# Kernel optimization log

Measured on AMD Instinct MI355X. Metric: run time of the kernel, lower is better.

The kernel has to match this reference:

```python
import jax, jax.numpy as jnp
import numpy as np

BS, NCAM, CIN, H, W = 1, 6, 512, 32, 88
MID = 256
DBINS = 112  # (58 - 2) / 0.5
VX, VY, VZ = 128, 128, 16


def conv2d(x, w, pad=1):
    return jax.lax.conv_general_dilated(
        x, w, (1, 1), [(pad, pad), (pad, pad)],
        dimension_numbers=('NCHW', 'OIHW', 'NCHW'))


def grid_sample_3d(feat, grid):
    """F.grid_sample 3D, bilinear, padding_mode='zeros', align_corners=False.
    feat: (N, C, D, H, W); grid: (N, X, Y, Z, 3) with xyz -> (W, H, D) coords in [-1,1].
    Returns (N, C, X, Y, Z)."""
    N, C, D, Hh, Ww = feat.shape
    gx, gy, gz = grid[..., 0], grid[..., 1], grid[..., 2]
    ix = ((gx + 1.0) * Ww - 1.0) * 0.5
    iy = ((gy + 1.0) * Hh - 1.0) * 0.5
    iz = ((gz + 1.0) * D - 1.0) * 0.5
    ix0, iy0, iz0 = jnp.floor(ix), jnp.floor(iy), jnp.floor(iz)
    fx, fy, fz = ix - ix0, iy - iy0, iz - iz0
    feat_flat = feat.reshape(N, C, D * Hh * Ww)
    out = jnp.zeros((N, C) + grid.shape[1:-1], feat.dtype)
    for dz in (0, 1):
        for dy in (0, 1):
            for dx in (0, 1):
                xi, yi, zi = ix0 + dx, iy0 + dy, iz0 + dz
                w_ = ((fx if dx else 1.0 - fx) * (fy if dy else 1.0 - fy)
                      * (fz if dz else 1.0 - fz))
                valid = ((xi >= 0) & (xi < Ww) & (yi >= 0) & (yi < Hh)
                         & (zi >= 0) & (zi < D))
                xc = jnp.clip(xi, 0, Ww - 1).astype(jnp.int32)
                yc = jnp.clip(yi, 0, Hh - 1).astype(jnp.int32)
                zc = jnp.clip(zi, 0, D - 1).astype(jnp.int32)
                idx = ((zc * Hh + yc) * Ww + xc).reshape(N, 1, -1)
                g = jnp.take_along_axis(feat_flat, idx, axis=2)
                g = g.reshape((N, C) + grid.shape[1:-1])
                out = out + g * (w_ * valid)[:, None]
    return out


def setup_inputs():
    key = jax.random.key(0)
    ks = jax.random.split(key, 16)
    f32 = jnp.float32
    img_feat = jax.random.normal(ks[0], (BS, NCAM, CIN, H, W), f32)
    intr = np.zeros((NCAM, 4, 4), np.float32)
    for i in range(NCAM):
        f = 1266.0 + 10.0 * i
        intr[i, 0, 0] = f; intr[i, 1, 1] = f
        intr[i, 0, 2] = 800.0; intr[i, 1, 2] = 450.0
        intr[i, 2, 2] = 1.0; intr[i, 3, 3] = 1.0
    intrins = jnp.asarray(intr)[None]  # (1, 6, 4, 4)
    # normalized frustum-sample coords; slightly beyond [-1,1] to hit zero padding
    grid = jax.random.uniform(ks[1], (BS, NCAM, VX, VY, VZ, 3), f32, -1.1, 1.1)
    s3 = (2.0 / (CIN * 9)) ** 0.5
    sm = (2.0 / (MID * 9)) ** 0.5
    s1 = (2.0 / MID) ** 0.5
    red_w = jax.random.normal(ks[2], (MID, CIN, 3, 3), f32) * s3
    red_s = jnp.ones((MID,), f32); red_b = jnp.zeros((MID,), f32)
    mlp_w1 = jax.random.normal(ks[3], (1, MID), f32) * 1.4
    mlp_b1 = jnp.zeros((MID,), f32)
    mlp_w2 = jax.random.normal(ks[4], (MID, MID), f32) * s1
    mlp_b2 = jnp.zeros((MID,), f32)
    se_rw = jax.random.normal(ks[5], (MID, MID, 1, 1), f32) * s1
    se_rb = jnp.zeros((MID,), f32)
    se_ew = jax.random.normal(ks[6], (MID, MID, 1, 1), f32) * s1
    se_eb = jnp.zeros((MID,), f32)
    bb_w = jax.random.normal(ks[7], (3, 2, MID, MID, 3, 3), f32) * sm
    bb_s = jnp.ones((3, 2, MID), f32); bb_b = jnp.zeros((3, 2, MID), f32)
    dp_w = jax.random.normal(ks[8], (DBINS, MID, 1, 1), f32) * s1
    dp_b = jnp.zeros((DBINS,), f32)
    return dict(img_feat=img_feat, intrins=intrins, grid=grid,
                red_w=red_w, red_s=red_s, red_b=red_b,
                mlp_w1=mlp_w1, mlp_b1=mlp_b1, mlp_w2=mlp_w2, mlp_b2=mlp_b2,
                se_rw=se_rw, se_rb=se_rb, se_ew=se_ew, se_eb=se_eb,
                bb_w=bb_w, bb_s=bb_s, bb_b=bb_b, dp_w=dp_w, dp_b=dp_b)


def reference(img_feat, intrins, grid, red_w, red_s, red_b,
              mlp_w1, mlp_b1, mlp_w2, mlp_b2,
              se_rw, se_rb, se_ew, se_eb, bb_w, bb_s, bb_b, dp_w, dp_b):
    bs, n, c, h, w = img_feat.shape
    x = img_feat.reshape(bs * n, c, h, w)
    # pixel-size SE conditioning from inverse intrinsics
    inv = jnp.linalg.inv(intrins)
    pixel_size = jnp.linalg.norm(
        jnp.stack([inv[..., 0, 0], inv[..., 1, 1]], -1), axis=-1).reshape(-1, 1)
    sp = pixel_size * 1000.0  # scale_depth_factor
    # reduce_conv: conv3x3 + (folded) BN + ReLU
    x = conv2d(x, red_w)
    x = jax.nn.relu(x * red_s[:, None, None] + red_b[:, None, None])
    # Mlp on scaled pixel size
    x_se = jax.nn.relu(sp @ mlp_w1 + mlp_b1) @ mlp_w2 + mlp_b2
    x_se = x_se[:, :, None, None]
    # SELayer
    t = jax.nn.relu(conv2d(x_se, se_rw, pad=0) + se_rb[:, None, None])
    gate = jax.nn.sigmoid(conv2d(t, se_ew, pad=0) + se_eb[:, None, None])
    x = x * gate
    # 3 BasicBlocks (conv-bn-relu-conv-bn + residual, relu), BN folded (eval)
    for i in range(3):
        y = conv2d(x, bb_w[i, 0])
        y = jax.nn.relu(y * bb_s[i, 0][:, None, None] + bb_b[i, 0][:, None, None])
        y = conv2d(y, bb_w[i, 1])
        y = y * bb_s[i, 1][:, None, None] + bb_b[i, 1][:, None, None]
        x = jax.nn.relu(x + y)
    depth = conv2d(x, dp_w, pad=0) + dp_b[:, None, None]  # (bs*n, D, h, w)
    dp = jax.nn.softmax(depth, axis=1)
    # stack depth prob and ones so one grid_sample yields features AND voxel mask
    feat = jnp.stack([dp, jnp.ones_like(dp)], axis=1)  # (bs*n, 2, D, h, w)
    g = grid.reshape((bs * n,) + grid.shape[2:])       # (bs*n, X, Y, Z, 3)
    sampled = grid_sample_3d(feat, g)                  # (bs*n, 2, X, Y, Z)
    sampled = sampled.reshape((bs, n) + sampled.shape[1:]).sum(axis=1)
    agg, masks = sampled[:, :1], sampled[:, 1:]
    out = jnp.where(masks > 0, agg / jnp.where(masks > 0, masks, 1.0), agg)
    return out  # (bs, 1, X, Y, Z)
```

## Files before the change

### kernel.cpp

```cpp
#include <hip/hip_runtime.h>

typedef _Float16 f16;
typedef _Float16 f16x8 __attribute__((ext_vector_type(8)));
typedef _Float16 f16x4 __attribute__((ext_vector_type(4)));
typedef float f32x4 __attribute__((ext_vector_type(4)));

#define NCAM 6
#define CINF 512
#define MIDC 256
#define DB   112
#define HH   32
#define WW   88
#define PH   34
#define PW   90
#define NPOS (HH*WW)

#define O_GATE   0L
#define O_WFRED  6144L
#define O_LOG    6144L
#define O_WFBB   2365440L
#define O_WFDP   9443328L
#define O_XP0    9508864L
#define O_X1     28309504L
#define O_DP     28309504L
#define O_X2     37709824L
#define O_X3     47110144L

__device__ __forceinline__ void gl_lds16(const void* g, void* l) {
  __builtin_amdgcn_global_load_lds((const __attribute__((address_space(1))) void*)g,
                                   (__attribute__((address_space(3))) void*)l, 16, 0, 0);
}

__global__ void halo_zero_kernel(f16* __restrict__ xp0, f16* __restrict__ X1,
                                 f16* __restrict__ X2, f16* __restrict__ X3) {
  int idx = blockIdx.x * 256 + threadIdx.x;
  f16* base; int C, rem;
  if (idx < 93696) { base = xp0; C = 512; rem = idx; }
  else {
    int k = idx - 93696;
    int bsel = k / 46848;
    if (bsel >= 3) return;
    rem = k - bsel * 46848; C = 256;
    base = (bsel == 0) ? X1 : (bsel == 1) ? X2 : X3;
  }
  int chunks = C >> 3;
  int cell = rem / chunks, cc = rem - cell * chunks;
  int cam = cell / 244, p = cell - cam * 244;
  int hh, ww;
  if (p < 90)       { hh = 0;  ww = p; }
  else if (p < 180) { hh = 33; ww = p - 90; }
  else { int q = p - 180; hh = 1 + (q >> 1); ww = (q & 1) * 89; }
  long o = ((long)(cam * PH + hh) * PW + ww) * C + cc * 8;
  f16x8 z = {0,0,0,0,0,0,0,0};
  *(f16x8*)(base + o) = z;
}

__global__ void wfrag_kernel(const float* __restrict__ src, const float* __restrict__ scale,
                             f16* __restrict__ dst, int NC, int G, int TAPS, int CI, int CO_SRC,
                             long per, long total) {
  long i = (long)blockIdx.x * blockDim.x + threadIdx.x;
  long stride = (long)gridDim.x * blockDim.x;
  int KST = CI >> 5;
  for (; i < total; i += stride) {
    int conv = (int)(i / per);
    long rem = i - (long)conv * per;
    int j = (int)(rem & 7);
    int lane = (int)((rem >> 3) & 63);
    int mi = (int)((rem >> 9) & 3);
    long b = rem >> 11;
    int ks = (int)(b % KST);
    long b2 = b / KST;
    int tap = (int)(b2 % TAPS);
    int g = (int)(b2 / TAPS);
    int co = g * 64 + mi * 16 + (lane & 15);
    int ci = ks * 32 + (lane >> 4) * 8 + j;
    float v = 0.f;
    if (co < CO_SRC) {
      v = src[(long)conv * CO_SRC * CI * TAPS + ((long)co * CI + ci) * TAPS + tap];
      if (scale) v *= scale[conv * CO_SRC + co];
    }
    dst[i] = (f16)v;
  }
}

__global__ void img_trans_kernel(const float* __restrict__ src, f16* __restrict__ dst) {
  __shared__ float tile[32][33];
  int tx = threadIdx.x & 31, ty = threadIdx.x >> 5;
  int wt = blockIdx.x % 3, ct = blockIdx.x / 3;
  int h = blockIdx.y, n = blockIdx.z;
  int w0 = wt * 32, c0 = ct * 32;
  #pragma unroll
  for (int i = 0; i < 4; ++i) {
    int cl = ty + i * 8;
    int w = w0 + tx;
    float v = 0.f;
    if (w < WW) v = src[((long)(n * CINF + c0 + cl) * HH + h) * WW + w];
    tile[cl][tx] = v;
  }
  __syncthreads();
  #pragma unroll
  for (int i = 0; i < 4; ++i) {
    int wl = ty + i * 8;
    int w = w0 + wl;
    if (w < WW)
      dst[((long)((n * PH + h + 1) * PW + (w + 1))) * CINF + c0 + tx] = (f16)tile[tx][wl];
  }
}

__global__ void se_gate_kernel(const float* __restrict__ intr,
                               const float* __restrict__ w1, const float* __restrict__ b1,
                               const float* __restrict__ w2, const float* __restrict__ b2,
                               const float* __restrict__ rw, const float* __restrict__ rb,
                               const float* __restrict__ ew, const float* __restrict__ eb,
                               float* __restrict__ gate) {
  __shared__ float sps;
  __shared__ float h1[MIDC];
  __shared__ float h2[MIDC];
  __shared__ float tt[MIDC];
  int n = blockIdx.x, c = threadIdx.x;
  if (c == 0) {
    float a[4][8];
    for (int i = 0; i < 4; ++i)
      for (int j = 0; j < 4; ++j) {
        a[i][j] = intr[n * 16 + i * 4 + j];
        a[i][4 + j] = (i == j) ? 1.f : 0.f;
      }
    for (int col = 0; col < 4; ++col) {
      int piv = col;
      for (int r2 = col + 1; r2 < 4; ++r2)
        if (fabsf(a[r2][col]) > fabsf(a[piv][col])) piv = r2;
      if (piv != col)
        for (int j = 0; j < 8; ++j) { float tv = a[col][j]; a[col][j] = a[piv][j]; a[piv][j] = tv; }
      float invp = 1.f / a[col][col];
      for (int j = 0; j < 8; ++j) a[col][j] *= invp;
      for (int r2 = 0; r2 < 4; ++r2)
        if (r2 != col) {
          float f = a[r2][col];
          for (int j = 0; j < 8; ++j) a[r2][j] -= f * a[col][j];
        }
    }
    float i00 = a[0][4], i11 = a[1][5];
    sps = sqrtf(i00 * i00 + i11 * i11) * 1000.f;
  }
  __syncthreads();
  float sp = sps;
  h1[c] = fmaxf(sp * w1[c] + b1[c], 0.f);
  __syncthreads();
  float acc = b2[c];
  for (int j = 0; j < MIDC; ++j) acc += h1[j] * w2[j * MIDC + c];
  h2[c] = acc;
  __syncthreads();
  acc = rb[c];
  for (int j = 0; j < MIDC; ++j) acc += rw[c * MIDC + j] * h2[j];
  tt[c] = fmaxf(acc, 0.f);
  __syncthreads();
  acc = eb[c];
  for (int j = 0; j < MIDC; ++j) acc += ew[c * MIDC + j] * tt[j];
  gate[n * MIDC + c] = 1.f / (1.f + expf(-acc));
}

template<int MODE, int CIN_T, int TAPS>
__global__ __launch_bounds__(256, 2)
void conv_mfma(const f16* __restrict__ X, const f16* __restrict__ Wf,
               const float* __restrict__ bias, const float* __restrict__ gate,
               const f16* __restrict__ res, f16* __restrict__ Yf16,
               float* __restrict__ Yf32, int co_tiles) {
  constexpr int KST = CIN_T / 32;
  constexpr int CPT = CIN_T / 64;
  constexpr int NCH = TAPS * CPT;
  constexpr int LCPT = (CPT == 8) ? 3 : 2;
  constexpr long GSTR = (long)TAPS * KST * 4096;
  constexpr int BSTR = 26624;
  __shared__ __align__(16) char S[2 * BSTR];

  const int t = threadIdx.x;
  const int wv = t >> 6, ln = t & 63, lm = ln & 15, quad = ln >> 4;
  const int wm = wv >> 1, wn = wv & 1;
  const int bid0 = blockIdx.x;
  const int cpx = gridDim.x >> 3;
  const int bid = (bid0 & 7) * cpx + (bid0 >> 3);
  const int co_tile = bid >> 8;
  const int r = bid & 255;
  int pbase, nrows;
  if (r < 224) { pbase = r * 64;               nrows = 64; }
  else         { pbase = 14336 + (r - 224) * 80; nrows = 80; }
  const int cam = pbase / NPOS;
  const int p0 = pbase - cam * NPOS;
  const int ntk = nrows >> 4;
  const int nregs = nrows >> 3;
  const int nti = (ntk + 1 - wn) >> 1;

  const f16* gB[3]; int ldsoffB[3];
  const int clog = (ln & 7) ^ (ln >> 3);
  #pragma unroll
  for (int j = 0; j < 3; ++j) {
    int reg = j * 4 + wv;
    int pl = p0 + reg * 8 + (ln >> 3);
    int hh = pl / WW, w2 = pl - hh * WW;
    gB[j] = X + ((long)((cam * PH + hh + 1) * PW + (w2 + 1))) * CIN_T + clog * 8;
    ldsoffB[j] = 16384 + reg * 1024;
  }

  const int sx0 = ((0 * 4 + quad) ^ (lm & 7)) * 16;
  const int sx1 = ((1 * 4 + quad) ^ (lm & 7)) * 16;

  f32x4 acc[4][3];
  #pragma unroll
  for (int mi = 0; mi < 4; ++mi)
    #pragma unroll
    for (int i = 0; i < 3; ++i)
      #pragma unroll
      for (int q = 0; q < 4; ++q) acc[mi][i][q] = 0.f;

  auto choff = [&](int c) -> long {
    long off = 0;
    if (TAPS == 9) {
      int tp = c >> LCPT;
      int dy = tp / 3 - 1, dx = tp % 3 - 1;
      off = (long)(dy * PW + dx) * CIN_T;
    }
    return off + (long)(c & (CPT - 1)) * 64;
  };
  auto stageA = [&](int bsel, int c) {
    const char* sb = (const char*)Wf + (long)c * 8192 + (long)ln * 16;
    char* db = S + bsel * BSTR;
    #pragma unroll
    for (int j = 0; j < 4; ++j) {
      int seg = j * 4 + wv;
      long gb = (long)(co_tile * 2 + (seg >> 3)) * GSTR;
      gl_lds16(sb + gb + (seg & 7) * 1024, db + seg * 1024);
    }
  };
  auto stageB = [&](int bsel, long curf) {
    #pragma unroll
    for (int j = 0; j < 3; ++j)
      if (j * 4 + wv < nregs)
        gl_lds16(gB[j] + curf, S + bsel * BSTR + ldsoffB[j]);
  };
  auto compute = [&](int bsel) {
    const char* ab = S + bsel * BSTR + wm * 8192 + ln * 16;
    const char* bb = S + bsel * BSTR + 16384 + lm * 128;
    #pragma unroll
    for (int s = 0; s < 2; ++s) {
      f16x8 af[4];
      #pragma unroll
      for (int mi = 0; mi < 4; ++mi)
        af[mi] = *(const f16x8*)(ab + s * 4096 + mi * 1024);
      int sx = s ? sx1 : sx0;
      #pragma unroll
      for (int i = 0; i < 3; ++i) {
        if (i < nti) {
          f16x8 bf = *(const f16x8*)(bb + (2 * i + wn) * 2048 + sx);
          #pragma unroll
          for (int mi = 0; mi < 4; ++mi)
            acc[mi][i] = __builtin_amdgcn_mfma_f32_16x16x32_f16(af[mi], bf, acc[mi][i], 0, 0, 0);
        }
      }
    }
  };

  stageA(0, 0);
  stageB(0, choff(0));
  __syncthreads();

  #pragma unroll 1
  for (int c = 0; c < NCH; ++c) {
    int cur = c & 1;
    if (c + 1 < NCH) { stageA(cur ^ 1, c + 1); stageB(cur ^ 1, choff(c + 1)); }
    compute(cur);
    __syncthreads();
  }

  float4 b4[4], g4[4];
  bool skip[4];
  #pragma unroll
  for (int mi = 0; mi < 4; ++mi) {
    int co_l = wm * 64 + mi * 16 + quad * 4;
    int co_g = co_tile * 128 + co_l;
    skip[mi] = (MODE == 3) && (co_l >= DB);
    if (!skip[mi]) b4[mi] = *(const float4*)(bias + co_g);
    if (MODE == 0) g4[mi] = *(const float4*)(gate + cam * MIDC + co_g);
  }
  #pragma unroll
  for (int i = 0; i < 3; ++i) {
    if (i >= nti) continue;
    int k = 2 * i + wn;
    int pos_l = p0 + k * 16 + lm;
    long ob;
    if (MODE == 3) ob = ((long)(cam * NPOS + pos_l)) * DB;
    else {
      int hh = pos_l / WW, w2 = pos_l - hh * WW;
      ob = ((long)((cam * PH + hh + 1) * PW + (w2 + 1))) * MIDC + co_tile * 128;
    }
    #pragma unroll
    for (int mi = 0; mi < 4; ++mi) {
      if (skip[mi]) continue;
      int co_l = wm * 64 + mi * 16 + quad * 4;
      float v[4];
      #pragma unroll
      for (int q = 0; q < 4; ++q) {
        float y = acc[mi][i][q];
        y += ((float*)&b4[mi])[q];
        if (MODE == 0) y = fmaxf(y, 0.f) * ((float*)&g4[mi])[q];
        else if (MODE == 1) y = fmaxf(y, 0.f);
        v[q] = y;
      }
      if (MODE == 3) {
        float4 o; o.x = v[0]; o.y = v[1]; o.z = v[2]; o.w = v[3];
        *(float4*)(Yf32 + ob + co_l) = o;
      } else if (MODE == 2) {
        f16x4 rv = *(const f16x4*)(res + ob + co_l);
        f16x4 o;
        #pragma unroll
        for (int q = 0; q < 4; ++q) o[q] = (f16)fmaxf(v[q] + (float)rv[q], 0.f);
        *(f16x4*)(Yf16 + ob + co_l) = o;
      } else {
        f16x4 o;
        #pragma unroll
        for (int q = 0; q < 4; ++q) o[q] = (f16)v[q];
        *(f16x4*)(Yf16 + ob + co_l) = o;
      }
    }
  }
}

__global__ void softmax_kernel(const float* __restrict__ L, float* __restrict__ dp) {
  int wid = (int)(((long)blockIdx.x * blockDim.x + threadIdx.x) >> 6);
  int lane = threadIdx.x & 63;
  if (wid >= NCAM * NPOS) return;
  const float* lp = L + (long)wid * DB;
  float v0 = -1e30f, v1 = -1e30f;
  if (lane < 56) { v0 = lp[lane * 2]; v1 = lp[lane * 2 + 1]; }
  float m = fmaxf(v0, v1);
  #pragma unroll
  for (int o = 32; o; o >>= 1) m = fmaxf(m, __shfl_xor(m, o));
  float e0 = 0.f, e1 = 0.f;
  if (lane < 56) { e0 = __expf(v0 - m); e1 = __expf(v1 - m); }
  float ssum = e0 + e1;
  #pragma unroll
  for (int o = 32; o; o >>= 1) ssum += __shfl_xor(ssum, o);
  float inv = 1.f / ssum;
  if (lane < 56) {
    float2 r; r.x = e0 * inv; r.y = e1 * inv;
    *(float2*)(dp + (long)wid * DB + lane * 2) = r;
  }
}

__global__ void sample_kernel(const float* __restrict__ grid, const float* __restrict__ dp,
                              float* __restrict__ out) {
  int v = blockIdx.x * blockDim.x + threadIdx.x;
  if (v >= 128 * 128 * 16) return;
  int vz = v & 15, vy = (v >> 4) & 127, vx = v >> 11;
  float agg = 0.f, msk = 0.f;
  #pragma unroll 1
  for (int n = 0; n < NCAM; ++n) {
    long gb = ((long)((n * 128 + vx) * 128 + vy) * 16 + vz) * 3;
    float gx = grid[gb], gy = grid[gb + 1], gz = grid[gb + 2];
    float ix = ((gx + 1.f) * (float)WW - 1.f) * 0.5f;
    float iy = ((gy + 1.f) * (float)HH - 1.f) * 0.5f;
    float iz = ((gz + 1.f) * (float)DB - 1.f) * 0.5f;
    float xf = floorf(ix), yf = floorf(iy), zf = floorf(iz);
    float fx = ix - xf, fy = iy - yf, fz = iz - zf;
    int x0 = (int)xf, y0 = (int)yf, z0 = (int)zf;
    float wxa[2] = {1.f - fx, fx};
    float wya[2] = {1.f - fy, fy};
    float wza[2] = {1.f - fz, fz};
    #pragma unroll
    for (int dy2 = 0; dy2 < 2; ++dy2) {
      int y = y0 + dy2;
      bool vyb = (y >= 0) && (y < HH);
      int yc = y < 0 ? 0 : (y > HH - 1 ? HH - 1 : y);
      #pragma unroll
      for (int dx2 = 0; dx2 < 2; ++dx2) {
        int x = x0 + dx2;
        bool vxb = (x >= 0) && (x < WW);
        int xc = x < 0 ? 0 : (x > WW - 1 ? WW - 1 : x);
        float wxy = wxa[dx2] * wya[dy2];
        const float* base = dp + ((long)((n * HH + yc) * WW + xc)) * DB;
        #pragma unroll
        for (int dz2 = 0; dz2 < 2; ++dz2) {
          int z = z0 + dz2;
          bool vzb = (z >= 0) && (z < DB);
          int zc = z < 0 ? 0 : (z > DB - 1 ? DB - 1 : z);
          float wgt = wxy * wza[dz2];
          if (vxb && vyb && vzb) {
            msk += wgt;
            agg += wgt * base[zc];
          }
        }
      }
    }
  }
  out[v] = (msk > 0.f) ? (agg / msk) : agg;
}

extern "C" void kernel_launch(void* const* d_in, const int* in_sizes, int n_in,
                              void* d_out, int out_size, void* d_ws, size_t ws_size,
                              hipStream_t stream) {
  const float* img   = (const float*)d_in[0];
  const float* intr  = (const float*)d_in[1];
  const float* grid  = (const float*)d_in[2];
  const float* red_w = (const float*)d_in[3];
  const float* red_s = (const float*)d_in[4];
  const float* red_b = (const float*)d_in[5];
  const float* w1    = (const float*)d_in[6];
  const float* b1    = (const float*)d_in[7];
  const float* w2    = (const float*)d_in[8];
  const float* b2    = (const float*)d_in[9];
  const float* rw    = (const float*)d_in[10];
  const float* rb    = (const float*)d_in[11];
  const float* ew    = (const float*)d_in[12];
  const float* eb    = (const float*)d_in[13];
  const float* bb_w  = (const float*)d_in[14];
  const float* bb_s  = (const float*)d_in[15];
  const float* bb_b  = (const float*)d_in[16];
  const float* dp_w  = (const float*)d_in[17];
  const float* dp_b  = (const float*)d_in[18];
  float* out = (float*)d_out;

  char* ws = (char*)d_ws;
  float* gate = (float*)(ws + O_GATE);
  f16* wfred  = (f16*)(ws + O_WFRED);
  f16* wfbb   = (f16*)(ws + O_WFBB);
  f16* wfdp   = (f16*)(ws + O_WFDP);
  f16* xp0    = (f16*)(ws + O_XP0);
  f16* X1     = (f16*)(ws + O_X1);
  f16* X2     = (f16*)(ws + O_X2);
  f16* X3     = (f16*)(ws + O_X3);
  float* Lg   = (float*)(ws + O_LOG);
  float* dpb  = (float*)(ws + O_DP);

  halo_zero_kernel<<<915, 256, 0, stream>>>(xp0, X1, X2, X3);
  {
    long per = 4L * 9 * 16 * 2048, total = per;
    wfrag_kernel<<<2048, 256, 0, stream>>>(red_w, red_s, wfred, 1, 4, 9, 512, 256, per, total);
  }
  {
    long per = 4L * 9 * 8 * 2048, total = 6 * per;
    wfrag_kernel<<<4096, 256, 0, stream>>>(bb_w, bb_s, wfbb, 6, 4, 9, 256, 256, per, total);
  }
  {
    long per = 2L * 1 * 8 * 2048, total = per;
    wfrag_kernel<<<128, 256, 0, stream>>>(dp_w, nullptr, wfdp, 1, 2, 1, 256, 112, per, total);
  }
  img_trans_kernel<<<dim3(48, 32, 6), 256, 0, stream>>>(img, xp0);
  se_gate_kernel<<<6, 256, 0, stream>>>(intr, w1, b1, w2, b2, rw, rb, ew, eb, gate);

  const long WCH = 4L * 9 * 8 * 2048;

  conv_mfma<0, 512, 9><<<512, 256, 0, stream>>>(xp0, wfred, red_b, gate, nullptr, X1, nullptr, 2);

  conv_mfma<1, 256, 9><<<512, 256, 0, stream>>>(X1, wfbb + 0 * WCH, bb_b + 0 * 256, nullptr, nullptr, X2, nullptr, 2);
  conv_mfma<2, 256, 9><<<512, 256, 0, stream>>>(X2, wfbb + 1 * WCH, bb_b + 1 * 256, nullptr, X1, X3, nullptr, 2);
  conv_mfma<1, 256, 9><<<512, 256, 0, stream>>>(X3, wfbb + 2 * WCH, bb_b + 2 * 256, nullptr, nullptr, X2, nullptr, 2);
  conv_mfma<2, 256, 9><<<512, 256, 0, stream>>>(X2, wfbb + 3 * WCH, bb_b + 3 * 256, nullptr, X3, X1, nullptr, 2);
  conv_mfma<1, 256, 9><<<512, 256, 0, stream>>>(X1, wfbb + 4 * WCH, bb_b + 4 * 256, nullptr, nullptr, X2, nullptr, 2);
  conv_mfma<2, 256, 9><<<512, 256, 0, stream>>>(X2, wfbb + 5 * WCH, bb_b + 5 * 256, nullptr, X1, X3, nullptr, 2);

  conv_mfma<3, 256, 1><<<256, 256, 0, stream>>>(X3, wfdp, dp_b, nullptr, nullptr, nullptr, Lg, 1);

  softmax_kernel<<<4224, 256, 0, stream>>>(Lg, dpb);
  sample_kernel<<<1024, 256, 0, stream>>>(grid, dpb, out);
}
```

Baseline: 492.2 us.

## Double conv pixel tile to 128-144 rows and halve grid size

Grows each conv block's pixel tile from 64/80 rows to 128/144 rows, so every weight tile staged in LDS is reused across twice as many output positions. Block count is halved and co_tile/row indexing is reordered so that both channel tiles of the same pixel tile are adjacent. The accumulator array grows to 4x5, and the launch-bounds occupancy hint is dropped. The cost is more registers and LDS per block, and with 256 blocks on 256 CUs only one block per CU, which leaves less latency hiding.

Result: slower. 526.9 us (+7.1%).

```diff
diff --git a/kernel.cpp b/kernel.cpp
--- a/kernel.cpp
+++ b/kernel.cpp
@@ -160,7 +160,7 @@
 }
 
 template<int MODE, int CIN_T, int TAPS>
-__global__ __launch_bounds__(256, 2)
+__global__ __launch_bounds__(256)
 void conv_mfma(const f16* __restrict__ X, const f16* __restrict__ Wf,
                const float* __restrict__ bias, const float* __restrict__ gate,
                const f16* __restrict__ res, f16* __restrict__ Yf16,
@@ -170,7 +170,7 @@
   constexpr int NCH = TAPS * CPT;
   constexpr int LCPT = (CPT == 8) ? 3 : 2;
   constexpr long GSTR = (long)TAPS * KST * 4096;
-  constexpr int BSTR = 26624;
+  constexpr int BSTR = 34816;
   __shared__ __align__(16) char S[2 * BSTR];
 
   const int t = threadIdx.x;
@@ -179,36 +179,39 @@
   const int bid0 = blockIdx.x;
   const int cpx = gridDim.x >> 3;
   const int bid = (bid0 & 7) * cpx + (bid0 >> 3);
-  const int co_tile = bid >> 8;
-  const int r = bid & 255;
-  int pbase, nrows;
-  if (r < 224) { pbase = r * 64;               nrows = 64; }
-  else         { pbase = 14336 + (r - 224) * 80; nrows = 80; }
-  const int cam = pbase / NPOS;
-  const int p0 = pbase - cam * NPOS;
+  const int co_tile = bid % co_tiles;
+  const int r = bid / co_tiles;
+  int cam, p0, nrows;
+  if (r < 44) { cam = r / 22; p0 = (r % 22) * 128; nrows = 128; }
+  else {
+    int rr = r - 44;
+    cam = 2 + rr / 21;
+    int q = rr % 21;
+    if (q < 13) { p0 = q * 128; nrows = 128; }
+    else        { p0 = 1664 + (q - 13) * 144; nrows = 144; }
+  }
   const int ntk = nrows >> 4;
   const int nregs = nrows >> 3;
   const int nti = (ntk + 1 - wn) >> 1;
 
-  const f16* gB[3]; int ldsoffB[3];
+  const f16* gB[5];
   const int clog = (ln & 7) ^ (ln >> 3);
   #pragma unroll
-  for (int j = 0; j < 3; ++j) {
-    int reg = j * 4 + wv;
-    int pl = p0 + reg * 8 + (ln >> 3);
+  for (int j = 0; j < 5; ++j) {
+    int seg = j * 4 + wv;
+    int pl = p0 + seg * 8 + (ln >> 3);
     int hh = pl / WW, w2 = pl - hh * WW;
     gB[j] = X + ((long)((cam * PH + hh + 1) * PW + (w2 + 1))) * CIN_T + clog * 8;
-    ldsoffB[j] = 16384 + reg * 1024;
   }
 
   const int sx0 = ((0 * 4 + quad) ^ (lm & 7)) * 16;
   const int sx1 = ((1 * 4 + quad) ^ (lm & 7)) * 16;
 
-  f32x4 acc[4][3];
+  f32x4 acc[4][5];
   #pragma unroll
   for (int mi = 0; mi < 4; ++mi)
     #pragma unroll
-    for (int i = 0; i < 3; ++i)
+    for (int i = 0; i < 5; ++i)
       #pragma unroll
       for (int q = 0; q < 4; ++q) acc[mi][i][q] = 0.f;
 
@@ -221,21 +224,22 @@
     }
     return off + (long)(c & (CPT - 1)) * 64;
   };
-  auto stageA = [&](int bsel, int c) {
+  auto stage = [&](int bsel, int c) {
+    char* db = S + bsel * BSTR;
     const char* sb = (const char*)Wf + (long)c * 8192 + (long)ln * 16;
-    char* db = S + bsel * BSTR;
     #pragma unroll
     for (int j = 0; j < 4; ++j) {
       int seg = j * 4 + wv;
       long gb = (long)(co_tile * 2 + (seg >> 3)) * GSTR;
       gl_lds16(sb + gb + (seg & 7) * 1024, db + seg * 1024);
     }
-  };
-  auto stageB = [&](int bsel, long curf) {
-    #pragma unroll
-    for (int j = 0; j < 3; ++j)
-      if (j * 4 + wv < nregs)
-        gl_lds16(gB[j] + curf, S + bsel * BSTR + ldsoffB[j]);
+    long curf = choff(c);
+    #pragma unroll
+    for (int j = 0; j < 5; ++j) {
+      int seg = j * 4 + wv;
+      if (seg < nregs)
+        gl_lds16(gB[j] + curf, db + 16384 + seg * 1024);
+    }
   };
   auto compute = [&](int bsel) {
     const char* ab = S + bsel * BSTR + wm * 8192 + ln * 16;
@@ -248,7 +252,7 @@
         af[mi] = *(const f16x8*)(ab + s * 4096 + mi * 1024);
       int sx = s ? sx1 : sx0;
       #pragma unroll
-      for (int i = 0; i < 3; ++i) {
+      for (int i = 0; i < 5; ++i) {
         if (i < nti) {
           f16x8 bf = *(const f16x8*)(bb + (2 * i + wn) * 2048 + sx);
           #pragma unroll
@@ -259,14 +263,13 @@
     }
   };
 
-  stageA(0, 0);
-  stageB(0, choff(0));
+  stage(0, 0);
   __syncthreads();
 
   #pragma unroll 1
   for (int c = 0; c < NCH; ++c) {
     int cur = c & 1;
-    if (c + 1 < NCH) { stageA(cur ^ 1, c + 1); stageB(cur ^ 1, choff(c + 1)); }
+    if (c + 1 < NCH) stage(cur ^ 1, c + 1);
     compute(cur);
     __syncthreads();
   }
@@ -282,7 +285,7 @@
     if (MODE == 0) g4[mi] = *(const float4*)(gate + cam * MIDC + co_g);
   }
   #pragma unroll
-  for (int i = 0; i < 3; ++i) {
+  for (int i = 0; i < 5; ++i) {
     if (i >= nti) continue;
     int k = 2 * i + wn;
     int pos_l = p0 + k * 16 + lm;
@@ -448,16 +451,16 @@
 
   const long WCH = 4L * 9 * 8 * 2048;
 
-  conv_mfma<0, 512, 9><<<512, 256, 0, stream>>>(xp0, wfred, red_b, gate, nullptr, X1, nullptr, 2);
-
-  conv_mfma<1, 256, 9><<<512, 256, 0, stream>>>(X1, wfbb + 0 * WCH, bb_b + 0 * 256, nullptr, nullptr, X2, nullptr, 2);
-  conv_mfma<2, 256, 9><<<512, 256, 0, stream>>>(X2, wfbb + 1 * WCH, bb_b + 1 * 256, nullptr, X1, X3, nullptr, 2);
-  conv_mfma<1, 256, 9><<<512, 256, 0, stream>>>(X3, wfbb + 2 * WCH, bb_b + 2 * 256, nullptr, nullptr, X2, nullptr, 2);
-  conv_mfma<2, 256, 9><<<512, 256, 0, stream>>>(X2, wfbb + 3 * WCH, bb_b + 3 * 256, nullptr, X3, X1, nullptr, 2);
-  conv_mfma<1, 256, 9><<<512, 256, 0, stream>>>(X1, wfbb + 4 * WCH, bb_b + 4 * 256, nullptr, nullptr, X2, nullptr, 2);
-  conv_mfma<2, 256, 9><<<512, 256, 0, stream>>>(X2, wfbb + 5 * WCH, bb_b + 5 * 256, nullptr, X1, X3, nullptr, 2);
-
-  conv_mfma<3, 256, 1><<<256, 256, 0, stream>>>(X3, wfdp, dp_b, nullptr, nullptr, nullptr, Lg, 1);
+  conv_mfma<0, 512, 9><<<256, 256, 0, stream>>>(xp0, wfred, red_b, gate, nullptr, X1, nullptr, 2);
+
+  conv_mfma<1, 256, 9><<<256, 256, 0, stream>>>(X1, wfbb + 0 * WCH, bb_b + 0 * 256, nullptr, nullptr, X2, nullptr, 2);
+  conv_mfma<2, 256, 9><<<256, 256, 0, stream>>>(X2, wfbb + 1 * WCH, bb_b + 1 * 256, nullptr, X1, X3, nullptr, 2);
+  conv_mfma<1, 256, 9><<<256, 256, 0, stream>>>(X3, wfbb + 2 * WCH, bb_b + 2 * 256, nullptr, nullptr, X2, nullptr, 2);
+  conv_mfma<2, 256, 9><<<256, 256, 0, stream>>>(X2, wfbb + 3 * WCH, bb_b + 3 * 256, nullptr, X3, X1, nullptr, 2);
+  conv_mfma<1, 256, 9><<<256, 256, 0, stream>>>(X1, wfbb + 4 * WCH, bb_b + 4 * 256, nullptr, nullptr, X2, nullptr, 2);
+  conv_mfma<2, 256, 9><<<256, 256, 0, stream>>>(X2, wfbb + 5 * WCH, bb_b + 5 * 256, nullptr, X1, X3, nullptr, 2);
+
+  conv_mfma<3, 256, 1><<<128, 256, 0, stream>>>(X3, wfdp, dp_b, nullptr, nullptr, nullptr, Lg, 1);
 
   softmax_kernel<<<4224, 256, 0, stream>>>(Lg, dpb);
   sample_kernel<<<1024, 256, 0, stream>>>(grid, dpb, out);
```
